# Optimization experiments

Hardware: AMD Instinct MI355X
Metric: run time of the kernel (lower is better)

## Reference

```python
import jax, jax.numpy as jnp
import numpy as np

B, TE, TD, HE, HD = 8, 256, 128, 512, 512


def setup_inputs() -> dict:
    key = jax.random.key(0)
    k1, k2, k3, k4, k5 = jax.random.split(key, 5)
    # scale weights down (original uses 'uniform' init) to keep tanh unsaturated
    return {
        "encoder_out_seq": jax.random.normal(k1, (B, TE, HE), dtype=jnp.float32),
        "decoder_out_seq": jax.random.normal(k2, (B, TD, HD), dtype=jnp.float32),
        "W_a": jax.random.normal(k3, (HE, HE), dtype=jnp.float32) * 0.05,
        "U_a": jax.random.normal(k4, (HD, HE), dtype=jnp.float32) * 0.05,
        "V_a": jax.random.normal(k5, (HE, 1), dtype=jnp.float32) * 0.05,
    }


def reference(encoder_out_seq, decoder_out_seq, W_a, U_a, V_a):
    # Bahdanau additive attention, vectorized over all decoder timesteps
    # (the original loops over Td via K.rnn; steps are independent).
    Ws = jnp.einsum('bte,eh->bth', encoder_out_seq, W_a)   # [B, Te, He]
    Uh = jnp.einsum('bdk,kh->bdh', decoder_out_seq, U_a)   # [B, Td, He]
    # tanh(S.Wa + h.Ua): broadcast to [B, Td, Te, He], contract with V_a
    act = jnp.tanh(Ws[:, None, :, :] + Uh[:, :, None, :])  # [B, Td, Te, He]
    e = jnp.einsum('bdth,ho->bdt', act, V_a)                # [B, Td, Te]
    e = jax.nn.softmax(e, axis=-1)                          # attention weights
    c = jnp.einsum('bdt,bth->bdh', e, encoder_out_seq)      # [B, Td, He] contexts
    return (c, e)
```

## Files before the change

### kernel.cpp

```cpp
#include <hip/hip_runtime.h>

#define B_  8
#define TE_ 256
#define TD_ 128
#define HE_ 512

typedef __attribute__((ext_vector_type(8))) short short8v;
typedef __attribute__((ext_vector_type(4))) float f32x4;

#define C2 2.8853900817779268f

__device__ __forceinline__ float wave_red_add(float s) {
#define DPPADD(CTRL) \
  s += __int_as_float(__builtin_amdgcn_update_dpp(0, __float_as_int(s), CTRL, 0xf, 0xf, true))
  DPPADD(0x111);
  DPPADD(0x112);
  DPPADD(0x114);
  DPPADD(0x118);
  DPPADD(0x142);
  DPPADD(0x143);
#undef DPPADD
  return s;
}

__global__ __launch_bounds__(512) void gemm_fused(
    const float* __restrict__ enc, const float* __restrict__ dec,
    const float* __restrict__ Wa, const float* __restrict__ Ua,
    float* __restrict__ C) {
  __shared__ short BT[2][32][512];
  const int bid = blockIdx.x;
  const int mt = bid % 24, nt = bid / 24;
  const int m0 = mt * 128, n0 = nt * 32;
  const bool isenc = (mt < 16);
  const float* Bsrc = isenc ? Wa : Ua;
  const float* Asrc = isenc ? enc + (size_t)m0 * 512
                            : dec + (size_t)(m0 - 2048) * 512;
  const int tid = threadIdx.x;
  {
    const int kp = tid >> 3;
    const int c4 = (tid & 7) * 4;
    for (int p = 0; p < 4; ++p) {
      const int k = 2 * kp + p * 128;
      float4 v0 = *(const float4*)(Bsrc + (size_t)k * 512 + n0 + c4);
      float4 v1 = *(const float4*)(Bsrc + (size_t)(k + 1) * 512 + n0 + c4);
      const float a0[4] = {v0.x, v0.y, v0.z, v0.w};
      const float a1[4] = {v1.x, v1.y, v1.z, v1.w};
      const int kc = k >> 3, klo = k & 7;
#pragma unroll
      for (int q = 0; q < 4; ++q) {
        const int n = c4 + q;
        unsigned u0 = __float_as_uint(a0[q]);
        unsigned u1 = __float_as_uint(a1[q]);
        unsigned hi32 = __builtin_amdgcn_perm(u1, u0, 0x07060302);
        float l0 = a0[q] - __uint_as_float(u0 & 0xffff0000u);
        float l1 = a1[q] - __uint_as_float(u1 & 0xffff0000u);
        unsigned lo32 = __builtin_amdgcn_perm(__float_as_uint(l1), __float_as_uint(l0), 0x07060302);
        const int slot = (kc & ~7) | ((kc ^ n) & 7);
        *(unsigned*)&BT[0][n][slot * 8 + klo] = hi32;
        *(unsigned*)&BT[1][n][slot * 8 + klo] = lo32;
      }
    }
  }
  __syncthreads();
  const int w = tid >> 6, lane = tid & 63;
  const int fm = lane & 15, fc = lane >> 4;
  const float* Ap = Asrc + (size_t)(w * 16 + fm) * 512 + fc * 8;
  f32x4 acc0 = {}, acc1 = {};
  float4 pfa[2], pfb[2];
  pfa[0] = *(const float4*)(Ap);
  pfb[0] = *(const float4*)(Ap + 4);
  pfa[1] = *(const float4*)(Ap + 32);
  pfb[1] = *(const float4*)(Ap + 36);
  for (int it = 0; it < 16; ++it) {
    const float4 fa = pfa[it & 1];
    const float4 fb = pfb[it & 1];
    if (it < 14) {
      pfa[it & 1] = *(const float4*)(Ap + (it + 2) * 32);
      pfb[it & 1] = *(const float4*)(Ap + (it + 2) * 32 + 4);
    }
    const float af[8] = {fa.x, fa.y, fa.z, fa.w, fb.x, fb.y, fb.z, fb.w};
    union { unsigned u[4]; short8v s; } ahu, alu;
#pragma unroll
    for (int e = 0; e < 4; ++e) {
      unsigned u0 = __float_as_uint(af[2 * e]);
      unsigned u1 = __float_as_uint(af[2 * e + 1]);
      ahu.u[e] = __builtin_amdgcn_perm(u1, u0, 0x07060302);
      float l0 = af[2 * e]     - __uint_as_float(u0 & 0xffff0000u);
      float l1 = af[2 * e + 1] - __uint_as_float(u1 & 0xffff0000u);
      alu.u[e] = __builtin_amdgcn_perm(__float_as_uint(l1), __float_as_uint(l0), 0x07060302);
    }
    const short8v ah = ahu.s, al = alu.s;
    const int kc = it * 4 + fc;
    const int base = kc & ~7;
    const int s0 = (base | ((kc ^ fm) & 7)) * 8;
    const int s1 = (base | ((kc ^ (16 + fm)) & 7)) * 8;
    short8v bh0 = *(const short8v*)&BT[0][fm][s0];
    short8v bl0 = *(const short8v*)&BT[1][fm][s0];
    short8v bh1 = *(const short8v*)&BT[0][16 + fm][s1];
    short8v bl1 = *(const short8v*)&BT[1][16 + fm][s1];
    acc0 = __builtin_amdgcn_mfma_f32_16x16x32_bf16(ah, bh0, acc0, 0, 0, 0);
    acc1 = __builtin_amdgcn_mfma_f32_16x16x32_bf16(ah, bh1, acc1, 0, 0, 0);
    acc0 = __builtin_amdgcn_mfma_f32_16x16x32_bf16(ah, bl0, acc0, 0, 0, 0);
    acc1 = __builtin_amdgcn_mfma_f32_16x16x32_bf16(ah, bl1, acc1, 0, 0, 0);
    acc0 = __builtin_amdgcn_mfma_f32_16x16x32_bf16(al, bh0, acc0, 0, 0, 0);
    acc1 = __builtin_amdgcn_mfma_f32_16x16x32_bf16(al, bh1, acc1, 0, 0, 0);
  }
  const int row = m0 + w * 16 + fc * 4;
  float* Cp = C + (size_t)row * 512 + n0 + fm;
#pragma unroll
  for (int r = 0; r < 4; ++r)
    Cp[(size_t)r * 512] = __builtin_amdgcn_exp2f(C2 * acc0[r]);
#pragma unroll
  for (int r = 0; r < 4; ++r)
    Cp[(size_t)r * 512 + 16] = __builtin_amdgcn_exp2f(C2 * acc1[r]);
}

__global__ __launch_bounds__(1024) void attn_fused(
    const float* __restrict__ EWs, const float* __restrict__ EU,
    const float* __restrict__ Va, float* __restrict__ e_out) {
  __shared__ float sEU[2][HE_];
  __shared__ float sV[HE_];
  __shared__ float sE[2][TE_];
  __shared__ float sRed[8];
  __shared__ float sNorm[2];
  const int tid = threadIdx.x;
  const int b  = blockIdx.x & 7;
  const int d0 = (blockIdx.x >> 3) * 2;
  if (tid < 256)
    ((float4*)sEU)[tid] = ((const float4*)(EU + (size_t)(b * TD_ + d0) * HE_))[tid];
  else if (tid < 384)
    ((float4*)sV)[tid - 256] = ((const float4*)Va)[tid - 256];
  __syncthreads();
  const int lane = tid & 63, w = tid >> 6;
  const int tb = w * 16;
  const int h0 = lane * 8;
  float eU[2][8], vv2[8], sumv = 0.f;
#pragma unroll
  for (int j = 0; j < 8; ++j) {
    const float vj = sV[h0 + j];
    sumv += vj;
    vv2[j] = 2.0f * vj;
    eU[0][j] = sEU[0][h0 + j];
    eU[1][j] = sEU[1][h0 + j];
  }
  const float* pw = EWs + ((size_t)b * TE_ + tb) * HE_ + h0;
  float4 a0 = *(const float4*)(pw);
  float4 a1 = *(const float4*)(pw + 4);
  float s0, s1;
#define TELT2(X, J) { \
    float E0 = (X) * eU[0][J]; \
    float E1 = (X) * eU[1][J]; \
    float r0 = __builtin_amdgcn_rcpf(E0 + 1.0f); \
    float r1 = __builtin_amdgcn_rcpf(E1 + 1.0f); \
    s0 = fmaf(-vv2[J], r0, s0); s1 = fmaf(-vv2[J], r1, s1); }
  for (int ti = 0; ti < 16; ++ti) {
    const float* pn = pw + HE_;
    float4 n0 = *(const float4*)(pn);
    float4 n1 = *(const float4*)(pn + 4);
    s0 = s1 = sumv;
    TELT2(a0.x, 0) TELT2(a0.y, 1) TELT2(a0.z, 2) TELT2(a0.w, 3)
    TELT2(a1.x, 4) TELT2(a1.y, 5) TELT2(a1.z, 6) TELT2(a1.w, 7)
    s0 = wave_red_add(s0);
    s1 = wave_red_add(s1);
    if (lane == 63) {
      sE[0][tb + ti] = s0;
      sE[1][tb + ti] = s1;
    }
    a0 = n0; a1 = n1;
    pw = pn;
  }
  __syncthreads();
  if (tid < 512) {
    const int dA = tid >> 8, t = tid & 255;
    const float ex = __expf(sE[dA][t]);
    float sum = wave_red_add(ex);
    if (lane == 63) sRed[w] = sum;
    __syncthreads();
    if (tid < 2)
      sNorm[tid] = 1.0f / (sRed[tid * 4] + sRed[tid * 4 + 1] + sRed[tid * 4 + 2] + sRed[tid * 4 + 3]);
    __syncthreads();
    e_out[(size_t)(b * TD_ + d0 + dA) * TE_ + t] = ex * sNorm[dA];
  } else {
    __syncthreads();
    __syncthreads();
  }
}

__global__ __launch_bounds__(512) void ctx_gemm(
    const float* __restrict__ e, const float* __restrict__ enc,
    float* __restrict__ c_out) {
  __shared__ short BT[2][32][256];
  const int bid = blockIdx.x;
  const int b = bid & 7, nt = bid >> 3;
  const int n0 = nt * 32;
  const float* A    = e   + (size_t)b * TD_ * TE_;
  const float* Bsrc = enc + (size_t)b * TE_ * HE_;
  const int tid = threadIdx.x;
  {
    const int kp = tid >> 3;
    const int c4 = (tid & 7) * 4;
    for (int p = 0; p < 2; ++p) {
      const int k = 2 * kp + p * 128;
      float4 v0 = *(const float4*)(Bsrc + (size_t)k * HE_ + n0 + c4);
      float4 v1 = *(const float4*)(Bsrc + (size_t)(k + 1) * HE_ + n0 + c4);
      const float a0[4] = {v0.x, v0.y, v0.z, v0.w};
      const float a1[4] = {v1.x, v1.y, v1.z, v1.w};
      const int kc = k >> 3, klo = k & 7;
#pragma unroll
      for (int q = 0; q < 4; ++q) {
        const int n = c4 + q;
        unsigned u0 = __float_as_uint(a0[q]);
        unsigned u1 = __float_as_uint(a1[q]);
        unsigned hi32 = __builtin_amdgcn_perm(u1, u0, 0x07060302);
        float l0 = a0[q] - __uint_as_float(u0 & 0xffff0000u);
        float l1 = a1[q] - __uint_as_float(u1 & 0xffff0000u);
        unsigned lo32 = __builtin_amdgcn_perm(__float_as_uint(l1), __float_as_uint(l0), 0x07060302);
        const int slot = (kc & ~7) | ((kc ^ n) & 7);
        *(unsigned*)&BT[0][n][slot * 8 + klo] = hi32;
        *(unsigned*)&BT[1][n][slot * 8 + klo] = lo32;
      }
    }
  }
  __syncthreads();
  const int w = tid >> 6, lane = tid & 63;
  const int fm = lane & 15, fc = lane >> 4;
  const float* Ap = A + (size_t)(w * 16 + fm) * TE_ + fc * 8;
  f32x4 acc0 = {}, acc1 = {};
  for (int it = 0; it < 8; ++it) {
    const float4 fa = *(const float4*)(Ap + it * 32);
    const float4 fb = *(const float4*)(Ap + it * 32 + 4);
    const float af[8] = {fa.x, fa.y, fa.z, fa.w, fb.x, fb.y, fb.z, fb.w};
    union { unsigned u[4]; short8v s; } ahu, alu;
#pragma unroll
    for (int q = 0; q < 4; ++q) {
      unsigned u0 = __float_as_uint(af[2 * q]);
      unsigned u1 = __float_as_uint(af[2 * q + 1]);
      ahu.u[q] = __builtin_amdgcn_perm(u1, u0, 0x07060302);
      float l0 = af[2 * q]     - __uint_as_float(u0 & 0xffff0000u);
      float l1 = af[2 * q + 1] - __uint_as_float(u1 & 0xffff0000u);
      alu.u[q] = __builtin_amdgcn_perm(__float_as_uint(l1), __float_as_uint(l0), 0x07060302);
    }
    const short8v ah = ahu.s, al = alu.s;
    const int kc = it * 4 + fc;
    const int base = kc & ~7;
    const int s0 = (base | ((kc ^ fm) & 7)) * 8;
    const int s1 = (base | ((kc ^ (16 + fm)) & 7)) * 8;
    short8v bh0 = *(const short8v*)&BT[0][fm][s0];
    short8v bl0 = *(const short8v*)&BT[1][fm][s0];
    short8v bh1 = *(const short8v*)&BT[0][16 + fm][s1];
    short8v bl1 = *(const short8v*)&BT[1][16 + fm][s1];
    acc0 = __builtin_amdgcn_mfma_f32_16x16x32_bf16(ah, bh0, acc0, 0, 0, 0);
    acc1 = __builtin_amdgcn_mfma_f32_16x16x32_bf16(ah, bh1, acc1, 0, 0, 0);
    acc0 = __builtin_amdgcn_mfma_f32_16x16x32_bf16(ah, bl0, acc0, 0, 0, 0);
    acc1 = __builtin_amdgcn_mfma_f32_16x16x32_bf16(ah, bl1, acc1, 0, 0, 0);
    acc0 = __builtin_amdgcn_mfma_f32_16x16x32_bf16(al, bh0, acc0, 0, 0, 0);
    acc1 = __builtin_amdgcn_mfma_f32_16x16x32_bf16(al, bh1, acc1, 0, 0, 0);
  }
  const int row = w * 16 + fc * 4;
  float* Cp = c_out + (size_t)(b * TD_ + row) * HE_ + n0 + fm;
#pragma unroll
  for (int r = 0; r < 4; ++r) Cp[(size_t)r * HE_] = acc0[r];
#pragma unroll
  for (int r = 0; r < 4; ++r) Cp[(size_t)r * HE_ + 16] = acc1[r];
}

extern "C" void kernel_launch(void* const* d_in, const int* in_sizes, int n_in,
                              void* d_out, int out_size, void* d_ws, size_t ws_size,
                              hipStream_t stream) {
  const float* enc = (const float*)d_in[0];
  const float* dec = (const float*)d_in[1];
  const float* Wa  = (const float*)d_in[2];
  const float* Ua  = (const float*)d_in[3];
  const float* Va  = (const float*)d_in[4];
  float* c_out = (float*)d_out;
  float* e_out = c_out + (size_t)B_ * TD_ * HE_;
  float* Cws = (float*)d_ws;
  const float* EWs = Cws;
  const float* EU  = Cws + (size_t)2048 * 512;
  gemm_fused<<<384, 512, 0, stream>>>(enc, dec, Wa, Ua, Cws);
  attn_fused<<<512, 1024, 0, stream>>>(EWs, EU, Va, e_out);
  ctx_gemm<<<128, 512, 0, stream>>>(e_out, enc, c_out);
}
```

Before: 110.0 us.

## Process four decoder steps per attention block with packed FMA and row reductions

The attention kernel now handles four decoder timesteps per block instead of two, which halves the grid and reuses each loaded EWs row across four outputs. The exp-product-plus-one step is computed with v_pk_fma_f32 on pairs. The per-row wave reduction is cut to a 16-lane row reduction, and the four partial sums are combined during the softmax phase. The aim is less global load traffic and fewer reduction instructions per element, at the cost of more registers and only 256 blocks, which may leave part of the GPU idle.

```diff
diff --git a/kernel.cpp b/kernel.cpp
--- a/kernel.cpp
+++ b/kernel.cpp
@@ -7,6 +7,7 @@
 
 typedef __attribute__((ext_vector_type(8))) short short8v;
 typedef __attribute__((ext_vector_type(4))) float f32x4;
+typedef __attribute__((ext_vector_type(2))) float f32x2;
 
 #define C2 2.8853900817779268f
 
@@ -21,6 +22,23 @@
   DPPADD(0x143);
 #undef DPPADD
   return s;
+}
+
+__device__ __forceinline__ float row_red_add(float s) {
+#define DPPADD(CTRL) \
+  s += __int_as_float(__builtin_amdgcn_update_dpp(0, __float_as_int(s), CTRL, 0xf, 0xf, true))
+  DPPADD(0x111);
+  DPPADD(0x112);
+  DPPADD(0x114);
+  DPPADD(0x118);
+#undef DPPADD
+  return s;
+}
+
+__device__ __forceinline__ f32x2 pk_fma(f32x2 a, f32x2 b, f32x2 c) {
+  f32x2 d;
+  asm("v_pk_fma_f32 %0, %1, %2, %3" : "=v"(d) : "v"(a), "v"(b), "v"(c));
+  return d;
 }
 
 __global__ __launch_bounds__(512) void gemm_fused(
@@ -118,72 +136,87 @@
 __global__ __launch_bounds__(1024) void attn_fused(
     const float* __restrict__ EWs, const float* __restrict__ EU,
     const float* __restrict__ Va, float* __restrict__ e_out) {
-  __shared__ float sEU[2][HE_];
+  __shared__ float sEU[4][HE_];
   __shared__ float sV[HE_];
-  __shared__ float sE[2][TE_];
-  __shared__ float sRed[8];
-  __shared__ float sNorm[2];
+  __shared__ float sE4[4][TE_][4];
+  __shared__ float sRed[16];
+  __shared__ float sNorm[4];
   const int tid = threadIdx.x;
   const int b  = blockIdx.x & 7;
-  const int d0 = (blockIdx.x >> 3) * 2;
-  if (tid < 256)
+  const int d0 = (blockIdx.x >> 3) * 4;
+  if (tid < 512)
     ((float4*)sEU)[tid] = ((const float4*)(EU + (size_t)(b * TD_ + d0) * HE_))[tid];
-  else if (tid < 384)
-    ((float4*)sV)[tid - 256] = ((const float4*)Va)[tid - 256];
+  else if (tid < 640)
+    ((float4*)sV)[tid - 512] = ((const float4*)Va)[tid - 512];
   __syncthreads();
   const int lane = tid & 63, w = tid >> 6;
   const int tb = w * 16;
   const int h0 = lane * 8;
-  float eU[2][8], vv2[8], sumv = 0.f;
+  f32x2 peU[4][4];
+  float vv2[8], sumv = 0.f;
 #pragma unroll
   for (int j = 0; j < 8; ++j) {
     const float vj = sV[h0 + j];
     sumv += vj;
     vv2[j] = 2.0f * vj;
-    eU[0][j] = sEU[0][h0 + j];
-    eU[1][j] = sEU[1][h0 + j];
-  }
+  }
+#pragma unroll
+  for (int d = 0; d < 4; ++d)
+#pragma unroll
+    for (int jj = 0; jj < 4; ++jj)
+      peU[d][jj] = ((const f32x2*)&sEU[d][h0])[jj];
+  const f32x2 one2 = {1.0f, 1.0f};
   const float* pw = EWs + ((size_t)b * TE_ + tb) * HE_ + h0;
-  float4 a0 = *(const float4*)(pw);
-  float4 a1 = *(const float4*)(pw + 4);
-  float s0, s1;
-#define TELT2(X, J) { \
-    float E0 = (X) * eU[0][J]; \
-    float E1 = (X) * eU[1][J]; \
-    float r0 = __builtin_amdgcn_rcpf(E0 + 1.0f); \
-    float r1 = __builtin_amdgcn_rcpf(E1 + 1.0f); \
-    s0 = fmaf(-vv2[J], r0, s0); s1 = fmaf(-vv2[J], r1, s1); }
+  f32x2 pX[4];
+#pragma unroll
+  for (int jj = 0; jj < 4; ++jj) pX[jj] = ((const f32x2*)pw)[jj];
   for (int ti = 0; ti < 16; ++ti) {
     const float* pn = pw + HE_;
-    float4 n0 = *(const float4*)(pn);
-    float4 n1 = *(const float4*)(pn + 4);
-    s0 = s1 = sumv;
-    TELT2(a0.x, 0) TELT2(a0.y, 1) TELT2(a0.z, 2) TELT2(a0.w, 3)
-    TELT2(a1.x, 4) TELT2(a1.y, 5) TELT2(a1.z, 6) TELT2(a1.w, 7)
-    s0 = wave_red_add(s0);
-    s1 = wave_red_add(s1);
-    if (lane == 63) {
-      sE[0][tb + ti] = s0;
-      sE[1][tb + ti] = s1;
-    }
-    a0 = n0; a1 = n1;
+    f32x2 nX[4];
+#pragma unroll
+    for (int jj = 0; jj < 4; ++jj) nX[jj] = ((const f32x2*)pn)[jj];
+    float s0 = sumv, s1 = sumv, s2 = sumv, s3 = sumv;
+#pragma unroll
+    for (int jj = 0; jj < 4; ++jj) {
+      const float va = vv2[2 * jj], vb = vv2[2 * jj + 1];
+      f32x2 e0 = pk_fma(pX[jj], peU[0][jj], one2);
+      f32x2 e1 = pk_fma(pX[jj], peU[1][jj], one2);
+      f32x2 e2 = pk_fma(pX[jj], peU[2][jj], one2);
+      f32x2 e3 = pk_fma(pX[jj], peU[3][jj], one2);
+      s0 = fmaf(-va, __builtin_amdgcn_rcpf(e0.x), s0);
+      s0 = fmaf(-vb, __builtin_amdgcn_rcpf(e0.y), s0);
+      s1 = fmaf(-va, __builtin_amdgcn_rcpf(e1.x), s1);
+      s1 = fmaf(-vb, __builtin_amdgcn_rcpf(e1.y), s1);
+      s2 = fmaf(-va, __builtin_amdgcn_rcpf(e2.x), s2);
+      s2 = fmaf(-vb, __builtin_amdgcn_rcpf(e2.y), s2);
+      s3 = fmaf(-va, __builtin_amdgcn_rcpf(e3.x), s3);
+      s3 = fmaf(-vb, __builtin_amdgcn_rcpf(e3.y), s3);
+    }
+    s0 = row_red_add(s0);
+    s1 = row_red_add(s1);
+    s2 = row_red_add(s2);
+    s3 = row_red_add(s3);
+    if ((lane & 15) == 15) {
+      const int r = lane >> 4;
+      sE4[0][tb + ti][r] = s0;
+      sE4[1][tb + ti][r] = s1;
+      sE4[2][tb + ti][r] = s2;
+      sE4[3][tb + ti][r] = s3;
+    }
+    pX[0] = nX[0]; pX[1] = nX[1]; pX[2] = nX[2]; pX[3] = nX[3];
     pw = pn;
   }
   __syncthreads();
-  if (tid < 512) {
-    const int dA = tid >> 8, t = tid & 255;
-    const float ex = __expf(sE[dA][t]);
-    float sum = wave_red_add(ex);
-    if (lane == 63) sRed[w] = sum;
-    __syncthreads();
-    if (tid < 2)
-      sNorm[tid] = 1.0f / (sRed[tid * 4] + sRed[tid * 4 + 1] + sRed[tid * 4 + 2] + sRed[tid * 4 + 3]);
-    __syncthreads();
-    e_out[(size_t)(b * TD_ + d0 + dA) * TE_ + t] = ex * sNorm[dA];
-  } else {
-    __syncthreads();
-    __syncthreads();
-  }
+  const int dA = tid >> 8, t = tid & 255;
+  const float* q = sE4[dA][t];
+  const float ex = __expf(q[0] + q[1] + q[2] + q[3]);
+  float sum = wave_red_add(ex);
+  if (lane == 63) sRed[w] = sum;
+  __syncthreads();
+  if (tid < 4)
+    sNorm[tid] = 1.0f / (sRed[tid * 4] + sRed[tid * 4 + 1] + sRed[tid * 4 + 2] + sRed[tid * 4 + 3]);
+  __syncthreads();
+  e_out[(size_t)(b * TD_ + d0 + dA) * TE_ + t] = ex * sNorm[dA];
 }
 
 __global__ __launch_bounds__(512) void ctx_gemm(
@@ -278,6 +311,6 @@
   const float* EWs = Cws;
   const float* EU  = Cws + (size_t)2048 * 512;
   gemm_fused<<<384, 512, 0, stream>>>(enc, dec, Wa, Ua, Cws);
-  attn_fused<<<512, 1024, 0, stream>>>(EWs, EU, Va, e_out);
+  attn_fused<<<256, 1024, 0, stream>>>(EWs, EU, Va, e_out);
   ctx_gemm<<<128, 512, 0, stream>>>(e_out, enc, c_out);
 }
```

Result: no change. 109.7 us (-0.3%).
